# Kernel optimization log

Measured on AMD Instinct MI355X. Metric: run time of the kernel, lower is better.

Reference implementation:

```python
import jax, jax.numpy as jnp
import numpy as np

N_CLASS = 20
N_SIGMA = 2
H = W = 512
B = 4
N_INST = 32
W_INST, W_VAR, W_SEED = 1.0, 10.0, 1.0
FG_WEIGHT = 10.0


def _xym():
    # channel 0: x along width, channel 1: y along height (matches torch buffer)
    xm = jnp.broadcast_to(jnp.linspace(0.0, 1.0, W)[None, :], (H, W))
    ym = jnp.broadcast_to(jnp.linspace(0.0, 1.0, H)[:, None], (H, W))
    return jnp.stack([xm, ym], axis=0)  # [2, H, W]


def lovasz_hinge_flat(logits, gt, valid):
    # logits, gt (0/1 float), valid (bool), all flat [P]; ignored pixels excluded
    P = logits.shape[0]
    vf = valid.astype(logits.dtype)
    signs = 2.0 * gt - 1.0
    # push ignored pixels to the end of the descending sort; relu(-1e9)=0 kills them
    errors = jnp.where(valid, 1.0 - logits * signs, -1e9)
    errors_sorted, perm = jax.lax.top_k(errors, P)  # descending
    gt_sorted = jnp.take(gt * vf, perm)
    v_sorted = jnp.take(vf, perm)
    gts = jnp.sum(gt * vf)
    inter = gts - jnp.cumsum(gt_sorted)
    union = gts + jnp.cumsum((1.0 - gt_sorted) * v_sorted)
    jac = 1.0 - inter / jnp.maximum(union, 1e-9)
    jac = jnp.concatenate([jac[:1], jac[1:] - jac[:-1]])
    return jnp.sum(jax.nn.relu(errors_sorted) * jac)


def _per_image(pred_b, inst_b, lab_b, xym, fg_w, n_inst):
    spatial_emb = jnp.tanh(pred_b[:2]) + xym            # [2,H,W]
    sigma = pred_b[2:2 + N_SIGMA]                       # [n_sigma,H,W]
    seed = jax.nn.sigmoid(pred_b[2 + N_SIGMA:2 + N_SIGMA + N_CLASS])  # [C,H,W]
    inst = inst_b[0]
    lab = lab_b[0]
    valid = (lab != 255)

    # background seed loss: sum over classes of seed^2 on pixels not of that class
    cls_ids = jnp.arange(N_CLASS)
    bg = (lab[None] != (cls_ids + 1)[:, None, None]) & valid[None]
    seed_bg = jnp.sum(jnp.square(seed) * bg)

    def per_inst(iid):
        m = (inst == iid)
        mf = m.astype(pred_b.dtype)
        cnt = jnp.maximum(jnp.sum(mf), 1.0)
        # to_center=True: center is mean coordinate of instance pixels
        center = jnp.sum(xym * mf[None], axis=(1, 2)) / cnt          # [2]
        s_mean = jnp.sum(sigma * mf[None], axis=(1, 2)) / cnt        # [n_sigma]
        var_l = jnp.sum(jnp.square(sigma - jax.lax.stop_gradient(s_mean)[:, None, None]) * mf[None]) / (N_SIGMA * cnt)
        s = jnp.exp(s_mean * 10.0)
        dist = jnp.exp(-jnp.sum(jnp.square(spatial_emb - center[:, None, None]) * s[:, None, None], axis=0))  # [H,W]
        inst_l = lovasz_hinge_flat((dist * 2.0 - 1.0).reshape(-1), mf.reshape(-1), valid.reshape(-1))
        cls = jnp.max(lab * m) - 1  # instance class (0-indexed)
        seed_c = jnp.take(seed, cls, axis=0)
        seed_fg = jnp.take(fg_w, cls) * jnp.sum(jnp.square(seed_c - jax.lax.stop_gradient(dist)) * mf)
        return inst_l, var_l, seed_fg

    inst_ls, var_ls, seed_fgs = jax.vmap(per_inst)(jnp.arange(1, n_inst + 1))
    instance_loss = jnp.sum(inst_ls) / n_inst
    var_loss = jnp.sum(var_ls) / n_inst
    seed_loss = (seed_bg + jnp.sum(seed_fgs)) / (H * W)
    return W_INST * instance_loss + W_VAR * var_loss + W_SEED * seed_loss


def setup_inputs() -> dict:
    key = jax.random.key(0)
    k1, k2 = jax.random.split(key)
    prediction = jax.random.normal(k1, (B, 2 + N_SIGMA + N_CLASS, H, W), dtype=jnp.float32)
    instances = jax.random.randint(k2, (B, 1, H, W), 0, N_INST + 1).astype(jnp.int32)
    # each instance id has a consistent class, as the torch instance_to_cls dict assumes
    labels = jnp.where(instances > 0, ((instances - 1) % N_CLASS) + 1, 0).astype(jnp.int32)
    return {"prediction": prediction, "instances": instances, "labels": labels, "n_instances": N_INST}


def reference(prediction, instances, labels, n_instances):
    xym = _xym()
    fg_w = jnp.full((N_CLASS,), FG_WEIGHT, dtype=prediction.dtype)
    per = jax.vmap(lambda p, i, l: _per_image(p, i, l, xym, fg_w, n_instances))(prediction, instances, labels)
    return jnp.mean(per) + jnp.sum(prediction) * 0.0
```

## Files before the change

### kernel.cpp

```cpp
#include <hip/hip_runtime.h>
#include <hip/hip_fp16.h>
#include <math.h>

#define HH 512
#define WW 512
#define BB 4
#define NCLS 20
#define NINST 32
#define NPIX (HH*WW)
#define NCH 24
#define NBIN 128
#define NCHUNK3 256
#define CPX3 1024
#define K3T 512
#define HSTR 33

#define OFF_PARTA  ((size_t)0)
#define OFF_PSEED  (OFF_PARTA + 256*256*4)
#define OFF_DER    (OFF_PSEED + 256*4)
#define OFF_SEEDBG (OFF_DER + 7*128*4)
#define OFF_INSTL  (OFF_SEEDBG + 4*4)
#define OFF_SFG    (OFF_INSTL + 128*4)
#define OFF_REC    ((OFF_SFG + 1024*4 + 255) & ~(size_t)255)
#define OFF_HIST   (OFF_REC + (size_t)BB*NPIX*8)

__device__ __forceinline__ float fast_rcp(float x) { return __builtin_amdgcn_rcpf(x); }
__device__ __forceinline__ float fast_sigmoid(float z) { return fast_rcp(1.0f + __expf(-z)); }
__device__ __forceinline__ float fast_tanh(float x) {
  return 1.0f - 2.0f * fast_rcp(__expf(2.0f * x) + 1.0f);
}

__global__ __launch_bounds__(256) void k1_stats(
    const float* __restrict__ pred, const int* __restrict__ inst,
    const int* __restrict__ lab,
    float* __restrict__ partA, float* __restrict__ partSeed,
    uint2* __restrict__ rec)
{
  __shared__ unsigned s_st[4][NINST][9];
  __shared__ float s_seed;
  int t = threadIdx.x;
  int w = t >> 6;
  for (int i = t; i < 4*NINST*9; i += 256) ((unsigned*)s_st)[i] = 0u;
  if (t == 0) s_seed = 0.f;
  __syncthreads();

  int b = blockIdx.x >> 6;
  int blk = blockIdx.x & 63;
  const float* pb = pred + (size_t)b*NCH*NPIX;
  float seedloc = 0.f;

  for (int r = 0; r < 4; ++r) {
    int p = blk*4096 + r*1024 + t*4;
    float4 e0v = *(const float4*)(pb + p);
    float4 e1v = *(const float4*)(pb + NPIX + p);
    float4 g0v = *(const float4*)(pb + 2*NPIX + p);
    float4 g1v = *(const float4*)(pb + 3*NPIX + p);
    int4 idv = *(const int4*)(inst + (size_t)b*NPIX + p);
    int4 lbv = *(const int4*)(lab + (size_t)b*NPIX + p);

    #pragma unroll
    for (int u = 0; u < 4; ++u) {
      int px = p + u;
      int x = px & (WW-1);
      int y = px >> 9;
      float xm = x * (1.0f/(WW-1));
      float ym = y * (1.0f/(HH-1));
      float g0 = (&g0v.x)[u];
      float g1 = (&g1v.x)[u];
      int id = (&idv.x)[u];
      int lb = (&lbv.x)[u];
      if (id >= 1) {
        int j = id - 1;
        unsigned* row = s_st[w][j];
        atomicAdd(&row[0], 1u | ((lb != 255) ? 0x10000u : 0u));
        atomicAdd((float*)&row[1], xm);
        atomicAdd((float*)&row[2], ym);
        atomicAdd((float*)&row[3], g0);
        atomicAdd((float*)&row[4], g1);
        atomicAdd((float*)&row[5], g0*g0);
        atomicAdd((float*)&row[6], g1*g1);
      }
    }

    float so[4] = {0.f,0.f,0.f,0.f};
    float Sv[4] = {0.f,0.f,0.f,0.f};
    for (int c = 0; c < NCLS; ++c) {
      float4 sv = *(const float4*)(pb + (size_t)(4+c)*NPIX + p);
      #pragma unroll
      for (int u = 0; u < 4; ++u) {
        float sg = fast_sigmoid((&sv.x)[u]);
        Sv[u] += sg*sg;
        if (c + 1 == (&lbv.x)[u]) so[u] = sg;
      }
    }
    #pragma unroll
    for (int u = 0; u < 4; ++u)
      if ((&lbv.x)[u] != 255) seedloc += Sv[u] - so[u]*so[u];

    uint2 r4[4];
    #pragma unroll
    for (int u = 0; u < 4; ++u) {
      int px = p + u;
      int x = px & (WW-1);
      int y = px >> 9;
      float ex = fast_tanh((&e0v.x)[u]) + x * (1.0f/(WW-1));
      float ey = fast_tanh((&e1v.x)[u]) + y * (1.0f/(HH-1));
      __half2 h = __floats2half2_rn(ex, ey);
      unsigned valid = ((&lbv.x)[u] != 255) ? 1u : 0u;
      unsigned meta = (unsigned)(&idv.x)[u] | (valid << 7);
      r4[u].x = *reinterpret_cast<unsigned*>(&h);
      r4[u].y = (unsigned)(unsigned char)(so[u]*255.f + 0.5f) | (meta << 8);
    }
    uint4* dst = (uint4*)(rec + (size_t)b*NPIX + p);
    dst[0] = make_uint4(r4[0].x, r4[0].y, r4[1].x, r4[1].y);
    dst[1] = make_uint4(r4[2].x, r4[2].y, r4[3].x, r4[3].y);
  }

  for (int o = 32; o; o >>= 1) seedloc += __shfl_down(seedloc, o);
  if ((t & 63) == 0) atomicAdd(&s_seed, seedloc);
  __syncthreads();

  if (t < 256) {
    int j = t & 31, f = t >> 5;
    float v;
    if (f == 0) {
      unsigned s = (s_st[0][j][0] & 0xFFFFu) + (s_st[1][j][0] & 0xFFFFu)
                 + (s_st[2][j][0] & 0xFFFFu) + (s_st[3][j][0] & 0xFFFFu);
      v = (float)s;
    } else if (f == 7) {
      unsigned s = (s_st[0][j][0] >> 16) + (s_st[1][j][0] >> 16)
                 + (s_st[2][j][0] >> 16) + (s_st[3][j][0] >> 16);
      v = (float)s;
    } else {
      v = __uint_as_float(s_st[0][j][f]) + __uint_as_float(s_st[1][j][f])
        + __uint_as_float(s_st[2][j][f]) + __uint_as_float(s_st[3][j][f]);
    }
    partA[(blockIdx.x << 8) + t] = v;
  }
  if (t == 0) partSeed[blockIdx.x] = s_seed;
}

__global__ __launch_bounds__(1024) void k2_reduce(
    const float* __restrict__ partA, const float* __restrict__ partSeed,
    float* __restrict__ der, float* __restrict__ seedbg)
{
  __shared__ float s_stats[8][128];
  int t = threadIdx.x;
  {
    int f = t >> 7, pair = t & 127;
    int b = pair >> 5, j = pair & 31;
    float s = 0.f;
    for (int blk = 0; blk < 64; ++blk)
      s += partA[((b*64 + blk) << 8) + (f << 5) + j];
    s_stats[f][pair] = s;
  }
  if (t < 4) {
    float ss = 0.f;
    for (int i = 0; i < 64; ++i) ss += partSeed[t*64 + i];
    seedbg[t] = ss;
  }
  __syncthreads();
  if (t < 128) {
    float cntA = s_stats[0][t];
    float cnt = fmaxf(cntA, 1.0f);
    float sumx = s_stats[1][t], sumy = s_stats[2][t];
    float s0 = s_stats[3][t], s1 = s_stats[4][t];
    float q0 = s_stats[5][t], q1 = s_stats[6][t];
    float Gv = s_stats[7][t];
    float cx = sumx/cnt, cy = sumy/cnt;
    float sm0 = s0/cnt, sm1 = s1/cnt;
    float varnum = q0 - 2.f*sm0*s0 + cntA*sm0*sm0
                 + q1 - 2.f*sm1*s1 + cntA*sm1*sm1;
    float varl = varnum / (2.0f * cnt);
    der[0*128+t] = cx;
    der[1*128+t] = cy;
    der[2*128+t] = -1.442695041f * expf(10.f*sm0);
    der[3*128+t] = -1.442695041f * expf(10.f*sm1);
    der[4*128+t] = varl;
    der[5*128+t] = Gv;
  }
}

__global__ __launch_bounds__(K3T) void k3_hist(
    const uint2* __restrict__ rec, const float* __restrict__ der,
    unsigned* __restrict__ hist, float* __restrict__ sfg)
{
  __shared__ unsigned hc[NBIN*HSTR];
  __shared__ float s_fg[8];
  int t = threadIdx.x;
  for (int i = t; i < NBIN*HSTR; i += K3T) hc[i] = 0u;
  int bid = blockIdx.x;
  int b = bid >> 8;
  int chunk = bid & 255;
  int w = t >> 6, lane = t & 63;
  int j = lane & 31, jp1 = j + 1;
  int pair = b*NINST + j;
  float cx = der[0*128+pair], cy = der[1*128+pair];
  float s0 = der[2*128+pair], s1 = der[3*128+pair];
  const uint2* rb = rec + (size_t)b*NPIX + chunk*CPX3 + w*128;
  __syncthreads();

  float fg = 0.f;
  #pragma unroll 4
  for (int r = 0; r < 64; ++r) {
    uint2 rv = rb[r*2 + (lane >> 5)];
    __half2 h;
    *reinterpret_cast<unsigned*>(&h) = rv.x;
    float2 e = __half22float2(h);
    unsigned hi = rv.y;
    float dx = e.x - cx, dy = e.y - cy;
    float dist = exp2f(dx*dx*s0 + dy*dy*s1);
    bool own = ((int)((hi >> 8) & 0x3F) == jp1);
    if (own) { float d = (float)(hi & 0xFFu)*(1.0f/255.f) - dist; fg += d*d; }
    if (hi & 0x8000u) {
      float f = own ? (1.0f - dist) : dist;
      unsigned bin = min((unsigned)(f * (float)NBIN), NBIN-1u);
      atomicAdd(&hc[bin*HSTR + j], own ? 0x10001u : 1u);
    }
  }
  for (int o = 32; o; o >>= 1) fg += __shfl_down(fg, o);
  if (lane == 0) s_fg[w] = fg;
  __syncthreads();
  if (t == 0) {
    float s = 0.f;
    #pragma unroll
    for (int i = 0; i < 8; ++i) s += s_fg[i];
    sfg[bid] = 10.0f * s;
  }
  unsigned* out = hist + (size_t)(b*NCHUNK3 + chunk) * (NINST*NBIN);
  #pragma unroll
  for (int k = 0; k < NINST*NBIN/K3T; ++k) {
    int idx = k*K3T + t;
    out[idx] = hc[(idx & 127)*HSTR + (idx >> 7)];
  }
}

__global__ __launch_bounds__(512) void k4_scan(
    const unsigned* __restrict__ hist, const float* __restrict__ der,
    float* __restrict__ instl)
{
  __shared__ unsigned s_c[4][NBIN], s_p[4][NBIN];
  int t = threadIdx.x;
  int pair = blockIdx.x;
  int b = pair >> 5, j = pair & 31;
  int grp = t >> 7, bin = t & 127;
  const unsigned* bp = hist + ((size_t)b*NCHUNK3*NINST + j)*NBIN + bin;
  unsigned c = 0, p = 0;
  #pragma unroll 8
  for (int ch = grp*64; ch < grp*64 + 64; ++ch) {
    unsigned v = bp[(size_t)ch * (NINST*NBIN)];
    c += v & 0xFFFFu; p += v >> 16;
  }
  s_c[grp][bin] = c; s_p[grp][bin] = p;
  __syncthreads();
  if (t < NBIN) {
    s_c[0][t] += s_c[1][t] + s_c[2][t] + s_c[3][t];
    s_p[0][t] += s_p[1][t] + s_p[2][t] + s_p[3][t];
  }
  __syncthreads();

  if (t < 64) {
    int lane = t;
    float G = der[5*128+pair];
    unsigned carryN = 0, carryP = 0;
    float Jprev = 0.f, L = 0.f;
    for (int c8 = 0; c8 < NBIN/64; ++c8) {
      int k = NBIN - 1 - c8*64 - lane;
      unsigned n = s_c[0][k], pp0 = s_p[0][k];
      for (int off = 1; off < 64; off <<= 1) {
        unsigned nn = __shfl_up(n, off);
        unsigned pq = __shfl_up(pp0, off);
        if (lane >= off) { n += nn; pp0 += pq; }
      }
      float fN = (float)(carryN + n);
      float fP = (float)(carryP + pp0);
      float uni = G + fN - fP;
      float J = 1.0f - (G - fP) / fmaxf(uni, 1e-9f);
      float Jp = __shfl_up(J, 1);
      if (lane == 0) Jp = Jprev;
      float v = (k + 0.5f) * (2.0f/NBIN);
      L += v * (J - Jp);
      carryN += __shfl(n, 63);
      carryP += __shfl(pp0, 63);
      Jprev  = __shfl(J, 63);
    }
    for (int o = 32; o; o >>= 1) L += __shfl_down(L, o);
    if (lane == 0) instl[pair] = L;
  }
}

__global__ __launch_bounds__(256) void k5_final(
    const float* __restrict__ instl, const float* __restrict__ der,
    const float* __restrict__ seedbg, const float* __restrict__ sfg,
    float* __restrict__ out)
{
  __shared__ float red[256];
  int t = threadIdx.x;
  float acc = 0.f;
  for (int i = t; i < 1024; i += 256) acc += sfg[i];
  acc *= (1.0f/NPIX);
  if (t < 4) acc += seedbg[t] * (1.0f/NPIX);
  if (t < 128) acc += (instl[t] + 10.0f*der[4*128+t]) * (1.0f/NINST);
  red[t] = acc; __syncthreads();
  for (int s = 128; s; s >>= 1) { if (t < s) red[t] += red[t+s]; __syncthreads(); }
  if (t == 0) out[0] = red[0] * (1.0f/BB);
}

extern "C" void kernel_launch(void* const* d_in, const int* in_sizes, int n_in,
                              void* d_out, int out_size, void* d_ws, size_t ws_size,
                              hipStream_t stream)
{
  const float* pred = (const float*)d_in[0];
  const int* inst = (const int*)d_in[1];
  const int* lab  = (const int*)d_in[2];
  char* ws = (char*)d_ws;
  float* partA = (float*)(ws + OFF_PARTA);
  float* partSeed = (float*)(ws + OFF_PSEED);
  float* der = (float*)(ws + OFF_DER);
  float* seedbg = (float*)(ws + OFF_SEEDBG);
  float* instl = (float*)(ws + OFF_INSTL);
  float* sfg = (float*)(ws + OFF_SFG);
  uint2* rec = (uint2*)(ws + OFF_REC);
  unsigned* hist = (unsigned*)(ws + OFF_HIST);

  hipLaunchKernelGGL(k1_stats, dim3(256), dim3(256), 0, stream,
                     pred, inst, lab, partA, partSeed, rec);
  hipLaunchKernelGGL(k2_reduce, dim3(1), dim3(1024), 0, stream,
                     partA, partSeed, der, seedbg);
  hipLaunchKernelGGL(k3_hist, dim3(BB*NCHUNK3), dim3(K3T), 0, stream,
                     rec, der, hist, sfg);
  hipLaunchKernelGGL(k4_scan, dim3(128), dim3(512), 0, stream, hist, der, instl);
  hipLaunchKernelGGL(k5_final, dim3(1), dim3(256), 0, stream,
                     instl, der, seedbg, sfg, (float*)d_out);
}
```

Measured before the change: 91.69 us.

## Spread stats kernel over more blocks and parallelize partial-sum reduction

The first statistics kernel now launches 1024 blocks that each handle 1024 pixels, instead of 256 blocks that each loop over four 1024-pixel chunks. This raises occupancy on the many compute units of the GPU for the bandwidth-bound pass over the 24-channel prediction tensor. Because there are four times as many per-block partials, the single-block reduction is split into a 32-block parallel reduction kernel followed by a small derive kernel. The cost is one extra kernel launch and more partial-sum traffic through global memory.

```diff
diff --git a/kernel.cpp b/kernel.cpp
--- a/kernel.cpp
+++ b/kernel.cpp
@@ -16,8 +16,9 @@
 #define HSTR 33
 
 #define OFF_PARTA  ((size_t)0)
-#define OFF_PSEED  (OFF_PARTA + 256*256*4)
-#define OFF_DER    (OFF_PSEED + 256*4)
+#define OFF_PSEED  (OFF_PARTA + 1024*256*4)
+#define OFF_STATS  (OFF_PSEED + 1024*4)
+#define OFF_DER    (OFF_STATS + 8*128*4)
 #define OFF_SEEDBG (OFF_DER + 7*128*4)
 #define OFF_INSTL  (OFF_SEEDBG + 4*4)
 #define OFF_SFG    (OFF_INSTL + 128*4)
@@ -44,59 +45,59 @@
   if (t == 0) s_seed = 0.f;
   __syncthreads();
 
-  int b = blockIdx.x >> 6;
-  int blk = blockIdx.x & 63;
+  int b = blockIdx.x >> 8;
+  int blk = blockIdx.x & 255;
   const float* pb = pred + (size_t)b*NCH*NPIX;
   float seedloc = 0.f;
 
-  for (int r = 0; r < 4; ++r) {
-    int p = blk*4096 + r*1024 + t*4;
-    float4 e0v = *(const float4*)(pb + p);
-    float4 e1v = *(const float4*)(pb + NPIX + p);
-    float4 g0v = *(const float4*)(pb + 2*NPIX + p);
-    float4 g1v = *(const float4*)(pb + 3*NPIX + p);
-    int4 idv = *(const int4*)(inst + (size_t)b*NPIX + p);
-    int4 lbv = *(const int4*)(lab + (size_t)b*NPIX + p);
-
+  int p = blk*1024 + t*4;
+  float4 e0v = *(const float4*)(pb + p);
+  float4 e1v = *(const float4*)(pb + NPIX + p);
+  float4 g0v = *(const float4*)(pb + 2*NPIX + p);
+  float4 g1v = *(const float4*)(pb + 3*NPIX + p);
+  int4 idv = *(const int4*)(inst + (size_t)b*NPIX + p);
+  int4 lbv = *(const int4*)(lab + (size_t)b*NPIX + p);
+
+  #pragma unroll
+  for (int u = 0; u < 4; ++u) {
+    int px = p + u;
+    int x = px & (WW-1);
+    int y = px >> 9;
+    float xm = x * (1.0f/(WW-1));
+    float ym = y * (1.0f/(HH-1));
+    float g0 = (&g0v.x)[u];
+    float g1 = (&g1v.x)[u];
+    int id = (&idv.x)[u];
+    int lb = (&lbv.x)[u];
+    if (id >= 1) {
+      int j = id - 1;
+      unsigned* row = s_st[w][j];
+      atomicAdd(&row[0], 1u | ((lb != 255) ? 0x10000u : 0u));
+      atomicAdd((float*)&row[1], xm);
+      atomicAdd((float*)&row[2], ym);
+      atomicAdd((float*)&row[3], g0);
+      atomicAdd((float*)&row[4], g1);
+      atomicAdd((float*)&row[5], g0*g0);
+      atomicAdd((float*)&row[6], g1*g1);
+    }
+  }
+
+  float so[4] = {0.f,0.f,0.f,0.f};
+  float Sv[4] = {0.f,0.f,0.f,0.f};
+  for (int c = 0; c < NCLS; ++c) {
+    float4 sv = *(const float4*)(pb + (size_t)(4+c)*NPIX + p);
     #pragma unroll
     for (int u = 0; u < 4; ++u) {
-      int px = p + u;
-      int x = px & (WW-1);
-      int y = px >> 9;
-      float xm = x * (1.0f/(WW-1));
-      float ym = y * (1.0f/(HH-1));
-      float g0 = (&g0v.x)[u];
-      float g1 = (&g1v.x)[u];
-      int id = (&idv.x)[u];
-      int lb = (&lbv.x)[u];
-      if (id >= 1) {
-        int j = id - 1;
-        unsigned* row = s_st[w][j];
-        atomicAdd(&row[0], 1u | ((lb != 255) ? 0x10000u : 0u));
-        atomicAdd((float*)&row[1], xm);
-        atomicAdd((float*)&row[2], ym);
-        atomicAdd((float*)&row[3], g0);
-        atomicAdd((float*)&row[4], g1);
-        atomicAdd((float*)&row[5], g0*g0);
-        atomicAdd((float*)&row[6], g1*g1);
-      }
-    }
-
-    float so[4] = {0.f,0.f,0.f,0.f};
-    float Sv[4] = {0.f,0.f,0.f,0.f};
-    for (int c = 0; c < NCLS; ++c) {
-      float4 sv = *(const float4*)(pb + (size_t)(4+c)*NPIX + p);
-      #pragma unroll
-      for (int u = 0; u < 4; ++u) {
-        float sg = fast_sigmoid((&sv.x)[u]);
-        Sv[u] += sg*sg;
-        if (c + 1 == (&lbv.x)[u]) so[u] = sg;
-      }
-    }
-    #pragma unroll
-    for (int u = 0; u < 4; ++u)
-      if ((&lbv.x)[u] != 255) seedloc += Sv[u] - so[u]*so[u];
-
+      float sg = fast_sigmoid((&sv.x)[u]);
+      Sv[u] += sg*sg;
+      if (c + 1 == (&lbv.x)[u]) so[u] = sg;
+    }
+  }
+  #pragma unroll
+  for (int u = 0; u < 4; ++u)
+    if ((&lbv.x)[u] != 255) seedloc += Sv[u] - so[u]*so[u];
+
+  {
     uint2 r4[4];
     #pragma unroll
     for (int u = 0; u < 4; ++u) {
@@ -120,7 +121,7 @@
   if ((t & 63) == 0) atomicAdd(&s_seed, seedloc);
   __syncthreads();
 
-  if (t < 256) {
+  {
     int j = t & 31, f = t >> 5;
     float v;
     if (f == 0) {
@@ -140,45 +141,55 @@
   if (t == 0) partSeed[blockIdx.x] = s_seed;
 }
 
-__global__ __launch_bounds__(1024) void k2_reduce(
-    const float* __restrict__ partA, const float* __restrict__ partSeed,
+__global__ __launch_bounds__(256) void k2a_reduce(
+    const float* __restrict__ partA, float* __restrict__ stats)
+{
+  __shared__ float red[256];
+  int bid = blockIdx.x;
+  int b = bid >> 3, f = bid & 7;
+  int t = threadIdx.x;
+  int j = t & 31, grp = t >> 5;
+  float s = 0.f;
+  #pragma unroll 8
+  for (int k = 0; k < 32; ++k) {
+    int blk = grp*32 + k;
+    s += partA[((b*256 + blk) << 8) + (f << 5) + j];
+  }
+  red[t] = s; __syncthreads();
+  for (int st = 128; st >= 32; st >>= 1) {
+    if (t < st) red[t] += red[t + st];
+    __syncthreads();
+  }
+  if (t < 32) stats[f*128 + b*32 + t] = red[t];
+}
+
+__global__ __launch_bounds__(128) void k2b_derive(
+    const float* __restrict__ stats, const float* __restrict__ partSeed,
     float* __restrict__ der, float* __restrict__ seedbg)
 {
-  __shared__ float s_stats[8][128];
-  int t = threadIdx.x;
-  {
-    int f = t >> 7, pair = t & 127;
-    int b = pair >> 5, j = pair & 31;
-    float s = 0.f;
-    for (int blk = 0; blk < 64; ++blk)
-      s += partA[((b*64 + blk) << 8) + (f << 5) + j];
-    s_stats[f][pair] = s;
-  }
+  int t = threadIdx.x;
   if (t < 4) {
     float ss = 0.f;
-    for (int i = 0; i < 64; ++i) ss += partSeed[t*64 + i];
+    for (int i = 0; i < 256; ++i) ss += partSeed[t*256 + i];
     seedbg[t] = ss;
   }
-  __syncthreads();
-  if (t < 128) {
-    float cntA = s_stats[0][t];
-    float cnt = fmaxf(cntA, 1.0f);
-    float sumx = s_stats[1][t], sumy = s_stats[2][t];
-    float s0 = s_stats[3][t], s1 = s_stats[4][t];
-    float q0 = s_stats[5][t], q1 = s_stats[6][t];
-    float Gv = s_stats[7][t];
-    float cx = sumx/cnt, cy = sumy/cnt;
-    float sm0 = s0/cnt, sm1 = s1/cnt;
-    float varnum = q0 - 2.f*sm0*s0 + cntA*sm0*sm0
-                 + q1 - 2.f*sm1*s1 + cntA*sm1*sm1;
-    float varl = varnum / (2.0f * cnt);
-    der[0*128+t] = cx;
-    der[1*128+t] = cy;
-    der[2*128+t] = -1.442695041f * expf(10.f*sm0);
-    der[3*128+t] = -1.442695041f * expf(10.f*sm1);
-    der[4*128+t] = varl;
-    der[5*128+t] = Gv;
-  }
+  float cntA = stats[0*128+t];
+  float cnt = fmaxf(cntA, 1.0f);
+  float sumx = stats[1*128+t], sumy = stats[2*128+t];
+  float s0 = stats[3*128+t], s1 = stats[4*128+t];
+  float q0 = stats[5*128+t], q1 = stats[6*128+t];
+  float Gv = stats[7*128+t];
+  float cx = sumx/cnt, cy = sumy/cnt;
+  float sm0 = s0/cnt, sm1 = s1/cnt;
+  float varnum = q0 - 2.f*sm0*s0 + cntA*sm0*sm0
+               + q1 - 2.f*sm1*s1 + cntA*sm1*sm1;
+  float varl = varnum / (2.0f * cnt);
+  der[0*128+t] = cx;
+  der[1*128+t] = cy;
+  der[2*128+t] = -1.442695041f * expf(10.f*sm0);
+  der[3*128+t] = -1.442695041f * expf(10.f*sm1);
+  der[4*128+t] = varl;
+  der[5*128+t] = Gv;
 }
 
 __global__ __launch_bounds__(K3T) void k3_hist(
@@ -316,6 +327,7 @@
   char* ws = (char*)d_ws;
   float* partA = (float*)(ws + OFF_PARTA);
   float* partSeed = (float*)(ws + OFF_PSEED);
+  float* stats = (float*)(ws + OFF_STATS);
   float* der = (float*)(ws + OFF_DER);
   float* seedbg = (float*)(ws + OFF_SEEDBG);
   float* instl = (float*)(ws + OFF_INSTL);
@@ -323,10 +335,11 @@
   uint2* rec = (uint2*)(ws + OFF_REC);
   unsigned* hist = (unsigned*)(ws + OFF_HIST);
 
-  hipLaunchKernelGGL(k1_stats, dim3(256), dim3(256), 0, stream,
+  hipLaunchKernelGGL(k1_stats, dim3(1024), dim3(256), 0, stream,
                      pred, inst, lab, partA, partSeed, rec);
-  hipLaunchKernelGGL(k2_reduce, dim3(1), dim3(1024), 0, stream,
-                     partA, partSeed, der, seedbg);
+  hipLaunchKernelGGL(k2a_reduce, dim3(32), dim3(256), 0, stream, partA, stats);
+  hipLaunchKernelGGL(k2b_derive, dim3(1), dim3(128), 0, stream,
+                     stats, partSeed, der, seedbg);
   hipLaunchKernelGGL(k3_hist, dim3(BB*NCHUNK3), dim3(K3T), 0, stream,
                      rec, der, hist, sfg);
   hipLaunchKernelGGL(k4_scan, dim3(128), dim3(512), 0, stream, hist, der, instl);
```

New measurement: 94.01 us. 1.03x slower.
